# Optimization experiments

Measured on AMD Instinct MI355X. Metric: run time of the kernel, lower is better.

## Reference

```python
import jax, jax.numpy as jnp
import numpy as np

B = 64
NS = [5024, 1257, 315, 80, 21]  # padded vertex counts per mesh level
K = 9                            # spiral length
LAT = 256


def _sconv(x, idx, W, b, elu=True):
    # x: [B, N, F], idx: [N, K] spiral neighbor indices -> gather, GEMM, activation, zero-pad mask
    Bq, N, _ = x.shape
    g = x[:, idx.reshape(-1), :].reshape(Bq, N, -1)  # [B, N, K*F]
    o = g @ W + b
    if elu:
        o = jax.nn.elu(o)
    return o.at[:, -1, :].set(0.0)  # zero the padding vertex


def _pool(M, x):
    # M: [M_out, M_in] dense down/up-sample matrix
    return jnp.einsum('mn,bnf->bmf', M, x)


def _forward(x, s0, s1, s2, s3, D0, D1, D2, D3, U0, U1, U2, U3,
             We0, be0, We1, be1, We2, be2, We3, be3,
             fceW, fceb, fcdW, fcdb,
             Wd0, bd0, Wd1, bd1, Wd2, bd2, Wd3, bd3):
    # encoder: spiral conv + downsample at each level
    h = _pool(D0, _sconv(x, s0, We0, be0))
    h = _pool(D1, _sconv(h, s1, We1, be1))
    h = _pool(D2, _sconv(h, s2, We2, be2))
    h = _pool(D3, _sconv(h, s3, We3, be3))
    z = h.reshape(h.shape[0], -1) @ fceW + fceb          # [B, LAT]
    # decoder: upsample + spiral conv, last conv has identity activation
    h = (z @ fcdW + fcdb).reshape(z.shape[0], NS[4], -1)  # [B, 21, 256]
    h = _sconv(_pool(U3, h), s3, Wd0, bd0)
    h = _sconv(_pool(U2, h), s2, Wd1, bd1)
    h = _sconv(_pool(U1, h), s1, Wd2, bd2)
    h = _sconv(_pool(U0, h), s0, Wd3, bd3, elu=False)
    return h  # [B, 5024, 3]


def setup_inputs() -> dict:
    key = jax.random.key(0)
    ks = iter(jax.random.split(key, 64))
    nrm = lambda shape, s=0.05: jax.random.normal(next(ks), shape, dtype=jnp.float32) * s
    d = {}
    d['x'] = jax.random.normal(next(ks), (B, NS[0], 3), dtype=jnp.float32)
    for i in range(4):
        n = NS[i]
        d[f's{i}'] = jax.random.randint(next(ks), (n, K), 0, n, dtype=jnp.int32).astype(jnp.int64)
    for i in range(4):
        d[f'D{i}'] = nrm((NS[i + 1], NS[i]))
        d[f'U{i}'] = nrm((NS[i], NS[i + 1]))
    enc = [(3, 64), (64, 64), (64, 128), (128, 256)]
    for i, (fi, fo) in enumerate(enc):
        d[f'We{i}'] = nrm((fi * K, fo))
        d[f'be{i}'] = jnp.zeros((fo,), jnp.float32)
    d['fceW'] = nrm((NS[4] * 256, LAT))
    d['fceb'] = jnp.zeros((LAT,), jnp.float32)
    d['fcdW'] = nrm((LAT, NS[4] * 256))
    d['fcdb'] = jnp.zeros((NS[4] * 256,), jnp.float32)
    dec = [(256, 128), (128, 64), (64, 64), (64, 3)]
    for i, (fi, fo) in enumerate(dec):
        d[f'Wd{i}'] = nrm((fi * K, fo))
        d[f'bd{i}'] = jnp.zeros((fo,), jnp.float32)
    return d


def reference(x, s0, s1, s2, s3, D0, D1, D2, D3, U0, U1, U2, U3,
              We0, be0, We1, be1, We2, be2, We3, be3,
              fceW, fceb, fcdW, fcdb,
              Wd0, bd0, Wd1, bd1, Wd2, bd2, Wd3, bd3):
    return _forward(x, s0, s1, s2, s3, D0, D1, D2, D3, U0, U1, U2, U3,
                    We0, be0, We1, be1, We2, be2, We3, be3,
                    fceW, fceb, fcdW, fcdb,
                    Wd0, bd0, Wd1, bd1, Wd2, bd2, Wd3, bd3)
```

## Files before the change

kernel.cpp:

```cpp
#include <hip/hip_runtime.h>
#include <math.h>

typedef __attribute__((ext_vector_type(8))) _Float16 half8;
typedef __attribute__((ext_vector_type(4))) float f32x4;
typedef unsigned long long u64;

#define BK 32

#define EPI_NAT  0
#define EPI_TR   1
#define EPI_FCD  2
#define EPI_OUT  3
#define EPI_PART 4

typedef const __attribute__((address_space(1))) void* gas1;
typedef __attribute__((address_space(3))) void* las3;

__device__ __forceinline__ void gl16(const void* g, void* l) {
    __builtin_amdgcn_global_load_lds((gas1)g, (las3)l, 16, 0, 0);
}
template<int N> __device__ __forceinline__ void vwait() {
    asm volatile("s_waitcnt vmcnt(%0)" :: "n"(N) : "memory");
}
__device__ __forceinline__ void barx() {
    asm volatile("" ::: "memory");
    __builtin_amdgcn_s_barrier();
    asm volatile("" ::: "memory");
}

__global__ __launch_bounds__(256, 3) void pool2_k(
    const _Float16* __restrict__ Aw, const _Float16* __restrict__ Bw,
    _Float16* __restrict__ Cp, int M, int Np, u64 c_rs)
{
    __shared__ _Float16 sA[2][128][BK];
    __shared__ _Float16 sB[2][128][BK];

    const int t  = threadIdx.x;
    const int m0 = blockIdx.y * 128;
    const int f0 = blockIdx.x * 128;
    const int lane = t & 63;
    const int wid  = t >> 6;
    const int wm = wid >> 1;
    const int wf = wid & 1;
    const int lm = lane & 15;
    const int lg = lane >> 4;

    f32x4 acc[4][4];
    #pragma unroll
    for (int i = 0; i < 4; ++i)
        #pragma unroll
        for (int j = 0; j < 4; ++j)
            acc[i][j] = (f32x4)0.0f;

    auto stage = [&](int buf, int ks) {
        #pragma unroll
        for (int j = 0; j < 2; ++j) {
            int c   = t + j * 256;
            int row = c >> 2;
            int sw  = ((c & 3) ^ ((row >> 1) & 3)) * 8;
            int rc  = m0 + row; if (rc >= M) rc = M - 1;
            gl16(Aw + (u64)rc * Np + ks * BK + sw,
                 (_Float16*)&sA[buf][0][0] + (u64)c * 8);
        }
        #pragma unroll
        for (int j = 0; j < 2; ++j) {
            int c   = t + j * 256;
            int row = c >> 2;
            int sw  = ((c & 3) ^ ((row >> 1) & 3)) * 8;
            gl16(Bw + (u64)(f0 + row) * Np + ks * BK + sw,
                 (_Float16*)&sB[buf][0][0] + (u64)c * 8);
        }
    };

    auto compute = [&](int buf) {
        const int sa = (lg ^ ((lm >> 1) & 3)) * 8;
        half8 af[4], bf[4];
        #pragma unroll
        for (int i = 0; i < 4; ++i)
            af[i] = *(const half8*)&sA[buf][wm * 64 + i * 16 + lm][sa];
        #pragma unroll
        for (int j = 0; j < 4; ++j)
            bf[j] = *(const half8*)&sB[buf][wf * 64 + j * 16 + lm][sa];
        #pragma unroll
        for (int i = 0; i < 4; ++i)
            #pragma unroll
            for (int j = 0; j < 4; ++j)
                acc[i][j] = __builtin_amdgcn_mfma_f32_16x16x32_f16(af[i], bf[j], acc[i][j], 0, 0, 0);
    };

    const int ke = Np / BK;
    stage(0, 0);
    int cur = 0;
    for (int ks = 0; ks < ke; ++ks) {
        if (ks + 1 < ke) { stage(cur ^ 1, ks + 1); vwait<4>(); }
        else             { vwait<0>(); }
        barx();
        compute(cur);
        barx();
        cur ^= 1;
    }

    #pragma unroll
    for (int j = 0; j < 4; ++j) {
        int fl = f0 + wf * 64 + j * 16 + lm;
        #pragma unroll
        for (int i = 0; i < 4; ++i) {
            #pragma unroll
            for (int r = 0; r < 4; ++r) {
                int m = m0 + wm * 64 + i * 16 + lg * 4 + r;
                if (m < M)
                    Cp[(u64)m * c_rs + fl] = (_Float16)acc[i][j][r];
            }
        }
    }
}

template<int AMODE, int EPI, int TBM, int TBF, int WM, int WF>
__global__ __launch_bounds__(256) void gemm_k(
    const _Float16* __restrict__ Aw, u64 a_rs,
    const int* __restrict__ idx, int FiLog,
    const _Float16* __restrict__ Bw,
    const float* __restrict__ bias,
    void* __restrict__ Cp, u64 c_rs, int Mp_out,
    int M, int Np, int F, int flags, int ksp)
{
    constexpr int FM = TBM / WM / 16;
    constexpr int FF = TBF / WF / 16;
    constexpr int LPS_A = TBM / 64;
    constexpr bool BSM = (TBF < 64);
    constexpr int LPS_B = BSM ? 0 : TBF / 64;
    constexpr int LW0 = LPS_A + (BSM ? 1 : LPS_B);
    constexpr int LWX = LPS_A + LPS_B;
    constexpr int NI = (AMODE == 1) ? TBM : 2;

    __shared__ _Float16 sA[3][TBM][BK];
    __shared__ _Float16 sB[3][TBF][BK];
    __shared__ int sIdx[NI][9];

    const int t  = threadIdx.x;
    const int b  = blockIdx.z;
    const int m0 = blockIdx.y * TBM;
    const int f0 = blockIdx.x * TBF;
    const int lane = t & 63;
    const int wid  = t >> 6;
    const int wm = wid / WF;
    const int wf = wid % WF;
    const int lm = lane & 15;
    const int lg = lane >> 4;
    const int Fi = 1 << FiLog;

    f32x4 acc[FM][FF];
    #pragma unroll
    for (int i = 0; i < FM; ++i)
        #pragma unroll
        for (int j = 0; j < FF; ++j)
            acc[i][j] = (f32x4)0.0f;

    if constexpr (AMODE == 1) {
        for (int i = t; i < TBM * 9; i += 256) {
            int r = i / 9, k = i - r * 9;
            int rc = m0 + r; if (rc >= M) rc = M - 1;
            sIdx[r][k] = idx[rc * 9 + k];
        }
        __syncthreads();
    } else if constexpr (AMODE == 5) {
        if (t < 18) {
            int r = t / 9, k = t - r * 9;
            sIdx[r][k] = idx[((m0 >> 6) + r) * 9 + k];
        }
        __syncthreads();
    }

    auto stage = [&](int buf, int ks) {
        if constexpr (AMODE != 2) {
            #pragma unroll
            for (int j = 0; j < LPS_A; ++j) {
                int c   = t + j * 256;
                int row = c >> 2;
                int sw  = ((c & 3) ^ ((row >> 1) & 3)) * 8;
                int col = ks * BK + sw;
                const _Float16* src;
                if constexpr (AMODE == 3) {
                    int rc = m0 + row; if (rc >= M) rc = M - 1;
                    src = Aw + (u64)rc * Np + col;
                } else if constexpr (AMODE == 1) {
                    int k = col >> FiLog, fi = col & (Fi - 1);
                    src = Aw + (u64)sIdx[row][k] * a_rs + b * Fi + fi;
                } else if constexpr (AMODE == 4) {
                    int k = col >> FiLog, fi = col & (Fi - 1);
                    src = Aw + (u64)k * a_rs + (m0 + row) * Fi + fi;
                } else {
                    int k = col >> FiLog, fi = col & (Fi - 1);
                    int bb = (m0 + row) & 63;
                    src = Aw + (u64)sIdx[row >> 6][k] * a_rs + bb * Fi + fi;
                }
                gl16(src, &sA[buf][row][(c & 3) * 8]);
            }
        }
        if constexpr (!BSM) {
            #pragma unroll
            for (int j = 0; j < LPS_B; ++j) {
                int c   = t + j * 256;
                int row = c >> 2;
                int sw  = ((c & 3) ^ ((row >> 1) & 3)) * 8;
                gl16(Bw + (u64)(f0 + row) * Np + ks * BK + sw, &sB[buf][row][(c & 3) * 8]);
            }
        } else {
            if (wid == 0) {
                int c   = t;
                int row = c >> 2;
                int sw  = ((c & 3) ^ ((row >> 1) & 3)) * 8;
                gl16(Bw + (u64)(f0 + row) * Np + ks * BK + sw, &sB[buf][row][(c & 3) * 8]);
            }
        }
    };

    auto compute = [&](int buf) {
        const int sa = (lg ^ ((lm >> 1) & 3)) * 8;
        half8 af[FM], bf[FF];
        #pragma unroll
        for (int i = 0; i < FM; ++i)
            af[i] = *(const half8*)&sA[buf][wm * (FM * 16) + i * 16 + lm][sa];
        #pragma unroll
        for (int j = 0; j < FF; ++j)
            bf[j] = *(const half8*)&sB[buf][wf * (FF * 16) + j * 16 + lm][sa];
        #pragma unroll
        for (int i = 0; i < FM; ++i)
            #pragma unroll
            for (int j = 0; j < FF; ++j)
                acc[i][j] = __builtin_amdgcn_mfma_f32_16x16x32_f16(af[i], bf[j], acc[i][j], 0, 0, 0);
    };

    if constexpr (AMODE == 2) {
        stage(0, 0);
        {
            int row = t >> 1;
            int base = (t & 1) * 16;
            int rg = m0 + row;
            #pragma unroll
            for (int q = 0; q < 16; ++q) {
                int n = base + q;
                _Float16 val = (_Float16)0.f;
                if (rg < M && n < 27) {
                    int k = n / 3, fi = n - k * 3;
                    val = Aw[(u64)idx[rg * 9 + k] * a_rs + b * 3 + fi];
                }
                int ch = (n >> 3) ^ ((row >> 1) & 3);
                sA[0][row][ch * 8 + (n & 7)] = val;
            }
        }
        __syncthreads();
        compute(0);
    } else {
        int kb = 0, ke = Np / BK;
        if constexpr (AMODE == 4) { kb = b * ksp; ke = kb + ksp; }
        stage(0, kb);
        if (kb + 1 < ke) stage(1, kb + 1);
        if (kb + 2 < ke) stage(2, kb + 2);
        int cur = 0;
        for (int ks = kb; ks < ke; ++ks) {
            int rem = ke - ks;
            if (rem >= 3) {
                if constexpr (LW0 == LWX) vwait<2 * LW0>();
                else { if (wid == 0) vwait<2 * LW0>(); else vwait<2 * LWX>(); }
            } else if (rem == 2) {
                if constexpr (LW0 == LWX) vwait<LW0>();
                else { if (wid == 0) vwait<LW0>(); else vwait<LWX>(); }
            } else {
                vwait<0>();
            }
            barx();
            compute(cur);
            barx();
            if (ks + 3 < ke) stage(cur, ks + 3);
            cur = (cur == 2) ? 0 : cur + 1;
        }
    }

    #pragma unroll
    for (int j = 0; j < FF; ++j) {
        int fl = f0 + wf * (FF * 16) + j * 16 + lm;
        float bv = 0.f;
        if (bias != nullptr && fl < F) bv = bias[fl];
        #pragma unroll
        for (int i = 0; i < FM; ++i) {
            #pragma unroll
            for (int r = 0; r < 4; ++r) {
                int m = m0 + wm * (FM * 16) + i * 16 + lg * 4 + r;
                float v = acc[i][j][r] + bv;
                if (flags & 1) v = (v > 0.f) ? v : expm1f(v);
                if constexpr (EPI == EPI_NAT) {
                    if (m < M && fl < F)
                        ((_Float16*)Cp)[(u64)m * c_rs + fl] = (_Float16)v;
                } else if constexpr (EPI == EPI_TR) {
                    if (m < Mp_out && fl < F) {
                        float o = (m < M && !((flags & 2) && m == M - 1)) ? v : 0.f;
                        ((_Float16*)Cp)[(u64)b * c_rs + (u64)fl * Mp_out + m] = (_Float16)o;
                    }
                } else if constexpr (EPI == EPI_FCD) {
                    if (m < M && fl < F)
                        ((_Float16*)Cp)[((u64)m * 256 + (fl & 255)) * 32 + (fl >> 8)] = (_Float16)v;
                } else if constexpr (EPI == EPI_PART) {
                    if (m < M && fl < F)
                        ((float*)Cp)[(u64)b * c_rs + (u64)m * F + fl] = v;
                } else {
                    if (m < M && fl < F) {
                        int vo = m >> 6, bb = m & 63;
                        float o = ((flags & 2) && vo == Mp_out - 1) ? 0.f : v;
                        ((float*)Cp)[((u64)bb * Mp_out + vo) * 3 + fl] = o;
                    }
                }
            }
        }
    }
}

struct CvtPtrs { const float* p[18]; };

constexpr int CV_R[18]  = {1257,5024,315,1257,80,315,21,80,  64,64,128,256,256,5376,128,64,64,16};
constexpr int CV_N[18]  = {5024,1257,1257,315,315,80,80,21,  27,576,576,1152,5376,256,2304,1152,576,576};
constexpr int CV_NP[18] = {5120,1280,1280,320,320,96,96,32,  32,576,576,1152,5376,256,2304,1152,576,576};
constexpr int CV_F[18]  = {0,0,0,0,0,0,0,0,  64,64,128,256,256,5376,128,64,64,3};

constexpr u64 cv_elems(int i) { return (u64)CV_R[i] * CV_NP[i]; }
constexpr u64 cv_off(int i) { u64 o = 0; for (int j = 0; j < i; ++j) o += (cv_elems(j) + 255) & ~(u64)255; return o; }
constexpr int cv_blk(int i) { return (int)((cv_elems(i) + 255) >> 8); }
constexpr int cv_start(int i) { int s = 0; for (int j = 0; j < i; ++j) s += cv_blk(j); return s; }

__global__ __launch_bounds__(256) void cvt_all(CvtPtrs ps, _Float16* __restrict__ dst)
{
    const int bx = blockIdx.x, t = threadIdx.x;
    #pragma unroll
    for (int i = 0; i < 18; ++i) {
        if (bx >= cv_start(i) && bx < cv_start(i + 1)) {
            const u64 e = (u64)(bx - cv_start(i)) * 256 + t;
            if (e < cv_elems(i)) {
                const int NP = CV_NP[i], N = CV_N[i], Fo = CV_F[i];
                int row = (int)(e / (u64)NP);
                int col = (int)(e - (u64)row * NP);
                float v = 0.f;
                const float* s = ps.p[i];
                if (Fo == 0) { if (col < N) v = s[(u64)row * N + col]; }
                else         { if (col < N && row < Fo) v = s[(u64)col * Fo + row]; }
                dst[cv_off(i) + e] = (_Float16)v;
            }
        }
    }
}

__global__ void cvt_x(const float* __restrict__ src, _Float16* __restrict__ dst)
{
    int i = blockIdx.x * 256 + threadIdx.x;
    if (i >= 64 * 5024 * 3) return;
    int v = i / 192;
    int r = i - v * 192;
    int b = r / 3, c = r - b * 3;
    dst[i] = (_Float16)src[((u64)b * 5024 + v) * 3 + c];
}

__global__ void reduce_fce(const float* __restrict__ part, const float* __restrict__ bias,
                           _Float16* __restrict__ z)
{
    int i = blockIdx.x * 256 + threadIdx.x;
    int fl = i & 255;
    float s = bias[fl];
    #pragma unroll
    for (int p = 0; p < 8; ++p) s += part[(u64)p * 16384 + i];
    z[i] = (_Float16)s;
}

extern "C" void kernel_launch(void* const* d_in, const int* in_sizes, int n_in,
                              void* d_out, int out_size, void* d_ws, size_t ws_size,
                              hipStream_t stream)
{
    const float* x  = (const float*)d_in[0];
    const int* s0 = (const int*)d_in[1];
    const int* s1 = (const int*)d_in[2];
    const int* s2 = (const int*)d_in[3];
    const int* s3 = (const int*)d_in[4];
    const float* be0 = (const float*)d_in[14];
    const float* be1 = (const float*)d_in[16];
    const float* be2 = (const float*)d_in[18];
    const float* be3 = (const float*)d_in[20];
    const float* fceb = (const float*)d_in[22];
    const float* fcdb = (const float*)d_in[24];
    const float* bd0 = (const float*)d_in[26];
    const float* bd1 = (const float*)d_in[28];
    const float* bd2 = (const float*)d_in[30];
    const float* bd3 = (const float*)d_in[32];

    _Float16* W = (_Float16*)d_ws;
    size_t off = 0;
    auto alloc = [&](size_t e) { size_t o = off; off += (e + 255) & ~(size_t)255; return o; };

    const size_t oActV = alloc((size_t)5024 * 4096);
    const size_t oActT = alloc((size_t)4096 * 5120);
    const size_t oZ    = alloc((size_t)64 * 256);
    const size_t oPart = alloc((size_t)8 * 64 * 256 * 2);
    const size_t oU3in = alloc((size_t)16384 * 32);
    const size_t oXp   = alloc((size_t)5024 * 192);
    const size_t oCvt  = alloc((size_t)(cv_off(17) + ((cv_elems(17) + 255) & ~(u64)255)));
    auto wofs = [&](int i) { return oCvt + (size_t)cv_off(i); };

    cvt_x<<<dim3((64 * 5024 * 3 + 255) / 256), 256, 0, stream>>>(x, W + oXp);
    {
        CvtPtrs ps;
        ps.p[0] = (const float*)d_in[5];
        ps.p[1] = (const float*)d_in[6];
        ps.p[2] = (const float*)d_in[7];
        ps.p[3] = (const float*)d_in[8];
        ps.p[4] = (const float*)d_in[9];
        ps.p[5] = (const float*)d_in[10];
        ps.p[6] = (const float*)d_in[11];
        ps.p[7] = (const float*)d_in[12];
        ps.p[8] = (const float*)d_in[13];
        ps.p[9] = (const float*)d_in[15];
        ps.p[10] = (const float*)d_in[17];
        ps.p[11] = (const float*)d_in[19];
        ps.p[12] = (const float*)d_in[21];
        ps.p[13] = (const float*)d_in[23];
        ps.p[14] = (const float*)d_in[25];
        ps.p[15] = (const float*)d_in[27];
        ps.p[16] = (const float*)d_in[29];
        ps.p[17] = (const float*)d_in[31];
        cvt_all<<<dim3(cv_start(18)), 256, 0, stream>>>(ps, W + oCvt);
    }
    hipMemsetAsync(W + oU3in, 0, (size_t)16384 * 32 * sizeof(_Float16), stream);

    #define GEMM(AM, EP, BM_, BF_, WM_, WF_, gx, gy, gz, Aw_, ars_, idx_, FiL_, Bw_, bias_, Cp_, crs_, Mp_, M_, Np_, F_, fl_, ksp_) \
        gemm_k<AM, EP, BM_, BF_, WM_, WF_><<<dim3(gx, gy, gz), 256, 0, stream>>>( \
            Aw_, ars_, idx_, FiL_, Bw_, bias_, Cp_, crs_, Mp_, M_, Np_, F_, fl_, ksp_)
    #define POOL(gx, gy, Aw_, Bw_, Cp_, M_, Np_, crs_) \
        pool2_k<<<dim3(gx, gy), 256, 0, stream>>>(Aw_, Bw_, Cp_, M_, Np_, crs_)

    GEMM(2, EPI_TR, 128, 64, 2, 2, 1, 40, 64, W + oXp, 192, s0, 0,
         W + wofs(8), be0, W + oActT, (u64)64 * 5120, 5120, 5024, 32, 64, 3, 0);
    POOL(32, 10, W + wofs(0), W + oActT, W + oActV, 1257, 5120, 4096);
    GEMM(1, EPI_TR, 128, 64, 2, 2, 1, 10, 64, W + oActV, 4096, s1, 6,
         W + wofs(9), be1, W + oActT, (u64)64 * 1280, 1280, 1257, 576, 64, 3, 0);
    POOL(32, 3, W + wofs(2), W + oActT, W + oActV, 315, 1280, 4096);
    GEMM(1, EPI_TR, 128, 64, 2, 2, 2, 3, 64, W + oActV, 4096, s2, 6,
         W + wofs(10), be2, W + oActT, (u64)128 * 320, 320, 315, 576, 128, 3, 0);
    POOL(64, 1, W + wofs(4), W + oActT, W + oActV, 80, 320, 8192);
    GEMM(1, EPI_TR, 128, 64, 2, 2, 4, 1, 64, W + oActV, 8192, s3, 7,
         W + wofs(11), be3, W + oActT, (u64)256 * 96, 96, 80, 1152, 256, 3, 0);
    POOL(128, 1, W + wofs(6), W + oActT, W + oActV, 21, 96, 16384);
    GEMM(4, EPI_PART, 64, 64, 2, 2, 4, 1, 8, W + oActV, 16384, nullptr, 8,
         W + wofs(12), nullptr, W + oPart, (u64)64 * 256, 0, 64, 5376, 256, 0, 21);
    reduce_fce<<<dim3(64), 256, 0, stream>>>((const float*)(W + oPart), fceb, W + oZ);
    GEMM(3, EPI_FCD, 64, 128, 2, 2, 42, 1, 1, W + oZ, 0, nullptr, 0,
         W + wofs(13), fcdb, W + oU3in, 0, 0, 64, 256, 5376, 0, 0);
    POOL(128, 1, W + wofs(7), W + oU3in, W + oActV, 80, 32, 16384);
    GEMM(1, EPI_TR, 128, 64, 2, 2, 2, 1, 64, W + oActV, 16384, s3, 8,
         W + wofs(14), bd0, W + oActT, (u64)128 * 96, 96, 80, 2304, 128, 3, 0);
    POOL(64, 3, W + wofs(5), W + oActT, W + oActV, 315, 96, 8192);
    GEMM(1, EPI_TR, 128, 64, 2, 2, 1, 3, 64, W + oActV, 8192, s2, 7,
         W + wofs(15), bd1, W + oActT, (u64)64 * 320, 320, 315, 1152, 64, 3, 0);
    POOL(32, 10, W + wofs(3), W + oActT, W + oActV, 1257, 320, 4096);
    GEMM(1, EPI_TR, 128, 64, 2, 2, 1, 10, 64, W + oActV, 4096, s1, 6,
         W + wofs(16), bd2, W + oActT, (u64)64 * 1280, 1280, 1257, 576, 64, 3, 0);
    POOL(32, 40, W + wofs(1), W + oActT, W + oActV, 5024, 1280, 4096);
    GEMM(5, EPI_OUT, 128, 16, 4, 1, 1, 2512, 1, W + oActV, 4096, s0, 6,
         W + wofs(17), bd3, d_out, 0, 5024, 321536, 576, 3, 2, 0);
    #undef GEMM
    #undef POOL
}
```

Before: 594.8 us.

## Triple-buffer pool GEMM loads and template M-tile to use smaller tiles

The pool GEMM kernel moves from double to triple buffering of shared-memory tiles, issuing loads two stages ahead and waiting with vmcnt counts matched to the number of loads per stage. It is also templated on the M tile height, and most pool launches now use 64-row tiles, doubling the grid to fill more compute units on the small mesh levels. The cost is more LDS per block, which may reduce occupancy, and a leftover unused forward declaration.

```diff
diff --git a/kernel.cpp b/kernel.cpp
--- a/kernel.cpp
+++ b/kernel.cpp
@@ -28,15 +28,21 @@
     asm volatile("" ::: "memory");
 }
 
+__global__ void __launch_bounds__(256, 3) pool2_k_impl();
+
+template<int TBM>
 __global__ __launch_bounds__(256, 3) void pool2_k(
     const _Float16* __restrict__ Aw, const _Float16* __restrict__ Bw,
     _Float16* __restrict__ Cp, int M, int Np, u64 c_rs)
 {
-    __shared__ _Float16 sA[2][128][BK];
-    __shared__ _Float16 sB[2][128][BK];
+    constexpr int FM  = TBM / 32;
+    constexpr int LPS = TBM / 64 + 2;
+
+    __shared__ _Float16 sA[3][TBM][BK];
+    __shared__ _Float16 sB[3][128][BK];
 
     const int t  = threadIdx.x;
-    const int m0 = blockIdx.y * 128;
+    const int m0 = blockIdx.y * TBM;
     const int f0 = blockIdx.x * 128;
     const int lane = t & 63;
     const int wid  = t >> 6;
@@ -45,16 +51,16 @@
     const int lm = lane & 15;
     const int lg = lane >> 4;
 
-    f32x4 acc[4][4];
-    #pragma unroll
-    for (int i = 0; i < 4; ++i)
+    f32x4 acc[FM][4];
+    #pragma unroll
+    for (int i = 0; i < FM; ++i)
         #pragma unroll
         for (int j = 0; j < 4; ++j)
             acc[i][j] = (f32x4)0.0f;
 
     auto stage = [&](int buf, int ks) {
         #pragma unroll
-        for (int j = 0; j < 2; ++j) {
+        for (int j = 0; j < TBM / 64; ++j) {
             int c   = t + j * 256;
             int row = c >> 2;
             int sw  = ((c & 3) ^ ((row >> 1) & 3)) * 8;
@@ -74,15 +80,15 @@
 
     auto compute = [&](int buf) {
         const int sa = (lg ^ ((lm >> 1) & 3)) * 8;
-        half8 af[4], bf[4];
-        #pragma unroll
-        for (int i = 0; i < 4; ++i)
-            af[i] = *(const half8*)&sA[buf][wm * 64 + i * 16 + lm][sa];
+        half8 af[FM], bf[4];
+        #pragma unroll
+        for (int i = 0; i < FM; ++i)
+            af[i] = *(const half8*)&sA[buf][wm * (FM * 16) + i * 16 + lm][sa];
         #pragma unroll
         for (int j = 0; j < 4; ++j)
             bf[j] = *(const half8*)&sB[buf][wf * 64 + j * 16 + lm][sa];
         #pragma unroll
-        for (int i = 0; i < 4; ++i)
+        for (int i = 0; i < FM; ++i)
             #pragma unroll
             for (int j = 0; j < 4; ++j)
                 acc[i][j] = __builtin_amdgcn_mfma_f32_16x16x32_f16(af[i], bf[j], acc[i][j], 0, 0, 0);
@@ -90,24 +96,29 @@
 
     const int ke = Np / BK;
     stage(0, 0);
+    if (1 < ke) stage(1, 1);
+    if (2 < ke) stage(2, 2);
     int cur = 0;
     for (int ks = 0; ks < ke; ++ks) {
-        if (ks + 1 < ke) { stage(cur ^ 1, ks + 1); vwait<4>(); }
-        else             { vwait<0>(); }
+        int rem = ke - ks;
+        if (rem >= 3)      vwait<2 * LPS>();
+        else if (rem == 2) vwait<LPS>();
+        else               vwait<0>();
         barx();
         compute(cur);
         barx();
-        cur ^= 1;
+        if (ks + 3 < ke) stage(cur, ks + 3);
+        cur = (cur == 2) ? 0 : cur + 1;
     }
 
     #pragma unroll
     for (int j = 0; j < 4; ++j) {
         int fl = f0 + wf * 64 + j * 16 + lm;
         #pragma unroll
-        for (int i = 0; i < 4; ++i) {
+        for (int i = 0; i < FM; ++i) {
             #pragma unroll
             for (int r = 0; r < 4; ++r) {
-                int m = m0 + wm * 64 + i * 16 + lg * 4 + r;
+                int m = m0 + wm * (FM * 16) + i * 16 + lg * 4 + r;
                 if (m < M)
                     Cp[(u64)m * c_rs + fl] = (_Float16)acc[i][j][r];
             }
@@ -430,36 +441,36 @@
     #define GEMM(AM, EP, BM_, BF_, WM_, WF_, gx, gy, gz, Aw_, ars_, idx_, FiL_, Bw_, bias_, Cp_, crs_, Mp_, M_, Np_, F_, fl_, ksp_) \
         gemm_k<AM, EP, BM_, BF_, WM_, WF_><<<dim3(gx, gy, gz), 256, 0, stream>>>( \
             Aw_, ars_, idx_, FiL_, Bw_, bias_, Cp_, crs_, Mp_, M_, Np_, F_, fl_, ksp_)
-    #define POOL(gx, gy, Aw_, Bw_, Cp_, M_, Np_, crs_) \
-        pool2_k<<<dim3(gx, gy), 256, 0, stream>>>(Aw_, Bw_, Cp_, M_, Np_, crs_)
+    #define POOL(TBM_, gx, gy, Aw_, Bw_, Cp_, M_, Np_, crs_) \
+        pool2_k<TBM_><<<dim3(gx, gy), 256, 0, stream>>>(Aw_, Bw_, Cp_, M_, Np_, crs_)
 
     GEMM(2, EPI_TR, 128, 64, 2, 2, 1, 40, 64, W + oXp, 192, s0, 0,
          W + wofs(8), be0, W + oActT, (u64)64 * 5120, 5120, 5024, 32, 64, 3, 0);
-    POOL(32, 10, W + wofs(0), W + oActT, W + oActV, 1257, 5120, 4096);
+    POOL(64, 32, 20, W + wofs(0), W + oActT, W + oActV, 1257, 5120, 4096);
     GEMM(1, EPI_TR, 128, 64, 2, 2, 1, 10, 64, W + oActV, 4096, s1, 6,
          W + wofs(9), be1, W + oActT, (u64)64 * 1280, 1280, 1257, 576, 64, 3, 0);
-    POOL(32, 3, W + wofs(2), W + oActT, W + oActV, 315, 1280, 4096);
+    POOL(64, 32, 5, W + wofs(2), W + oActT, W + oActV, 315, 1280, 4096);
     GEMM(1, EPI_TR, 128, 64, 2, 2, 2, 3, 64, W + oActV, 4096, s2, 6,
          W + wofs(10), be2, W + oActT, (u64)128 * 320, 320, 315, 576, 128, 3, 0);
-    POOL(64, 1, W + wofs(4), W + oActT, W + oActV, 80, 320, 8192);
+    POOL(64, 64, 2, W + wofs(4), W + oActT, W + oActV, 80, 320, 8192);
     GEMM(1, EPI_TR, 128, 64, 2, 2, 4, 1, 64, W + oActV, 8192, s3, 7,
          W + wofs(11), be3, W + oActT, (u64)256 * 96, 96, 80, 1152, 256, 3, 0);
-    POOL(128, 1, W + wofs(6), W + oActT, W + oActV, 21, 96, 16384);
+    POOL(64, 128, 1, W + wofs(6), W + oActT, W + oActV, 21, 96, 16384);
     GEMM(4, EPI_PART, 64, 64, 2, 2, 4, 1, 8, W + oActV, 16384, nullptr, 8,
          W + wofs(12), nullptr, W + oPart, (u64)64 * 256, 0, 64, 5376, 256, 0, 21);
     reduce_fce<<<dim3(64), 256, 0, stream>>>((const float*)(W + oPart), fceb, W + oZ);
     GEMM(3, EPI_FCD, 64, 128, 2, 2, 42, 1, 1, W + oZ, 0, nullptr, 0,
          W + wofs(13), fcdb, W + oU3in, 0, 0, 64, 256, 5376, 0, 0);
-    POOL(128, 1, W + wofs(7), W + oU3in, W + oActV, 80, 32, 16384);
+    POOL(64, 128, 2, W + wofs(7), W + oU3in, W + oActV, 80, 32, 16384);
     GEMM(1, EPI_TR, 128, 64, 2, 2, 2, 1, 64, W + oActV, 16384, s3, 8,
          W + wofs(14), bd0, W + oActT, (u64)128 * 96, 96, 80, 2304, 128, 3, 0);
-    POOL(64, 3, W + wofs(5), W + oActT, W + oActV, 315, 96, 8192);
+    POOL(64, 64, 5, W + wofs(5), W + oActT, W + oActV, 315, 96, 8192);
     GEMM(1, EPI_TR, 128, 64, 2, 2, 1, 3, 64, W + oActV, 8192, s2, 7,
          W + wofs(15), bd1, W + oActT, (u64)64 * 320, 320, 315, 1152, 64, 3, 0);
-    POOL(32, 10, W + wofs(3), W + oActT, W + oActV, 1257, 320, 4096);
+    POOL(64, 32, 20, W + wofs(3), W + oActT, W + oActV, 1257, 320, 4096);
     GEMM(1, EPI_TR, 128, 64, 2, 2, 1, 10, 64, W + oActV, 4096, s1, 6,
          W + wofs(16), bd2, W + oActT, (u64)64 * 1280, 1280, 1257, 576, 64, 3, 0);
-    POOL(32, 40, W + wofs(1), W + oActT, W + oActV, 5024, 1280, 4096);
+    POOL(128, 32, 40, W + wofs(1), W + oActT, W + oActV, 5024, 1280, 4096);
     GEMM(5, EPI_OUT, 128, 16, 4, 1, 1, 2512, 1, W + oActV, 4096, s0, 6,
          W + wofs(17), bd3, d_out, 0, 5024, 321536, 576, 3, 2, 0);
     #undef GEMM
```

Result: faster. 572.2 us (-3.8%).
